# Performance work log

Measured on AMD Instinct MI355X. Metric: run time of the kernel, lower is better.

Reference implementation:

```python
import jax, jax.numpy as jnp
import numpy as np

D_MODEL = 1024
H = 16
D_K = D_MODEL // H


def setup_inputs() -> dict:
    key = jax.random.key(0)
    ks = jax.random.split(key, 12)
    B, S = 2, 2048
    scale = 1.0 / np.sqrt(D_MODEL)
    inp = {
        "q": jax.random.normal(ks[0], (B, S, D_MODEL), jnp.float32),
        "k": jax.random.normal(ks[1], (B, S, D_MODEL), jnp.float32),
        "v": jax.random.normal(ks[2], (B, S, D_MODEL), jnp.float32),
        "mask": jnp.ones((B, 1, S, S), jnp.int32),
        "w_q": jax.random.normal(ks[3], (D_MODEL, D_MODEL), jnp.float32) * scale,
        "b_q": jnp.zeros((D_MODEL,), jnp.float32),
        "w_k": jax.random.normal(ks[4], (D_MODEL, D_MODEL), jnp.float32) * scale,
        "b_k": jnp.zeros((D_MODEL,), jnp.float32),
        "w_v": jax.random.normal(ks[5], (D_MODEL, D_MODEL), jnp.float32) * scale,
        "b_v": jnp.zeros((D_MODEL,), jnp.float32),
        "w_o": jax.random.normal(ks[6], (D_MODEL, D_MODEL), jnp.float32) * scale,
        "b_o": jnp.zeros((D_MODEL,), jnp.float32),
    }
    return inp


def _split_heads(x):
    B, S, _ = x.shape
    return x.reshape(B, S, H, D_K).transpose(0, 2, 1, 3)  # [B,H,S,Dk]


def reference(q, k, v, mask, w_q, b_q, w_k, b_k, w_v, b_v, w_o, b_o):
    # Linear projections (torch Linear: x @ W^T + b)
    query = _split_heads(q @ w_q.T + b_q)
    key = _split_heads(k @ w_k.T + b_k)
    value = _split_heads(v @ w_v.T + b_v)

    # scaled dot-product attention: [B,H,S,S]
    scores = jnp.einsum("bhqd,bhkd->bhqk", query, key) / jnp.sqrt(
        jnp.asarray(D_K, query.dtype)
    )
    scores = jnp.where(mask == 0, jnp.asarray(-1e9, scores.dtype), scores)
    attn = jax.nn.softmax(scores, axis=-1)  # dropout p=0.0 -> identity
    out = jnp.einsum("bhqk,bhkd->bhqd", attn, value)  # [B,H,S,Dk]

    # combine heads -> [B,S,D_MODEL]
    B = out.shape[0]
    out = out.transpose(0, 2, 1, 3).reshape(B, -1, D_MODEL)
    return out @ w_o.T + b_o
```

## Files before the change

### kernel.cpp

```cpp
#include <hip/hip_runtime.h>
#include <hip/hip_bf16.h>

#define S_LEN 2048
#define BATCH 2
#define NH    16
#define DK    64
#define DM    1024

typedef __bf16 bf16x8 __attribute__((ext_vector_type(8)));
typedef float  f32x4  __attribute__((ext_vector_type(4)));
typedef ushort u16x8  __attribute__((ext_vector_type(8)));

__device__ __forceinline__ float bf2f(ushort u) {
    union { unsigned int i; float f; } v; v.i = ((unsigned int)u) << 16; return v.f;
}
__device__ __forceinline__ ushort f2bf(float f) {
    union { float f; unsigned int i; } v; v.f = f;
    unsigned int u = v.i;
    unsigned int r = u + 0x7fff + ((u >> 16) & 1);
    return (ushort)(r >> 16);
}
__device__ __forceinline__ unsigned int packbf(float a, float b) {
    union { float f; unsigned int u; } x, y; x.f = a; y.f = b;
    return (x.u >> 16) | (y.u & 0xFFFF0000u);
}

__device__ __forceinline__ void async_copy16(const ushort* g, ushort* l) {
    __builtin_amdgcn_global_load_lds(
        (__attribute__((address_space(1))) void*)(g),
        (__attribute__((address_space(3))) void*)(l), 16, 0, 0);
}

__global__ void detect(const ushort* __restrict__ q, int* __restrict__ flags) {
    __shared__ int red[256];
    int tid = threadIdx.x;
    int cnt = 0;
    for (int i = tid; i < 2048; i += 256) {
        ushort e = q[2 * i];
        int ex = (e >> 7) & 0xFF;
        if (ex == 0 || (ex >= 107 && ex <= 147)) cnt++;
    }
    red[tid] = cnt;
    __syncthreads();
    for (int s = 128; s > 0; s >>= 1) {
        if (tid < s) red[tid] += red[tid + s];
        __syncthreads();
    }
    if (tid == 0) {
        flags[0] = (red[0] < 1229) ? 1 : 0;
        flags[1] = 0;
    }
}

__global__ void mask_check(const int* __restrict__ mask, int* __restrict__ flags) {
    const int total = BATCH * S_LEN * S_LEN / 4;
    int idx = blockIdx.x * blockDim.x + threadIdx.x;
    int stride = gridDim.x * blockDim.x;
    bool bad = false;
    for (int i = idx; i < total; i += stride) {
        int4 v = ((const int4*)mask)[i];
        if (v.x == 0 || v.y == 0 || v.z == 0 || v.w == 0) bad = true;
    }
    if (__any(bad)) {
        if ((threadIdx.x & 63) == 0) atomicOr(&flags[1], 1);
    }
}

#define NJOBS 11
struct CvtJobs { const void* src[NJOBS]; };

__device__ __constant__ const int g_cum[NJOBS + 1] = {
    0, 4194304, 8388608, 12582912, 13631488, 14680064, 15728640,
    16777216, 16778240, 16779264, 16780288, 16781312
};

__global__ __launch_bounds__(256) void convert_all(CvtJobs J, ushort* __restrict__ conv,
                                                   const int* __restrict__ flags) {
    bool isf32 = flags[0] != 0;
    const int total_chunks = 16781312 / 8;
    int c = blockIdx.x * blockDim.x + threadIdx.x;
    int stride = gridDim.x * blockDim.x;
    for (; c < total_chunks; c += stride) {
        int e = c * 8;
        int j = 0;
        while (j + 1 < NJOBS + 1 && e >= g_cum[j + 1]) j++;
        int local = e - g_cum[j];
        if (isf32) {
            const float* s = (const float*)J.src[j] + local;
            f32x4 a = *(const f32x4*)s;
            f32x4 b = *(const f32x4*)(s + 4);
            ushort o[8] = { f2bf(a[0]), f2bf(a[1]), f2bf(a[2]), f2bf(a[3]),
                            f2bf(b[0]), f2bf(b[1]), f2bf(b[2]), f2bf(b[3]) };
            *(ushort4*)&conv[e]     = *(ushort4*)&o[0];
            *(ushort4*)&conv[e + 4] = *(ushort4*)&o[4];
        } else {
            const ushort* s = (const ushort*)J.src[j] + local;
            bf16x8 v = *(const bf16x8*)s;
            *(bf16x8*)&conv[e] = v;
        }
    }
}

struct GArg { const ushort* x; const ushort* w; const ushort* bias; void* y; int split; float scale; };

__global__ __launch_bounds__(256) void gemm_bt(GArg a0, GArg a1, GArg a2,
                                               const int* __restrict__ flags) {
    GArg A = (blockIdx.z == 0) ? a0 : (blockIdx.z == 1 ? a1 : a2);
    const int K = 1024, N = 1024;
    __shared__ ushort As[2][128 * 32];
    __shared__ ushort Bs[2][128 * 32];

    int tid = threadIdx.x;
    int w = tid >> 6, lane = tid & 63;
    int wm = (w >> 1) * 64, wn = (w & 1) * 64;

    int id = blockIdx.x + 8 * blockIdx.y;
    int m0 = (id & 31) * 128;
    int n0 = (id >> 5) * 128;

    f32x4 acc[4][4] = {};

    int srow0 = w * 16 + (lane >> 2);
    int srow1 = (w + 4) * 16 + (lane >> 2);
    int schunk = ((lane & 3) ^ ((lane >> 3) & 3)) * 8;

    int fr = lane & 15;
    int qd = lane >> 4;
    int fcp = (qd ^ ((fr >> 1) & 3)) * 8;

    const ushort* xr0 = A.x + (size_t)(m0 + srow0) * K + schunk;
    const ushort* xr1 = A.x + (size_t)(m0 + srow1) * K + schunk;
    const ushort* wr0 = A.w + (size_t)(n0 + srow0) * K + schunk;
    const ushort* wr1 = A.w + (size_t)(n0 + srow1) * K + schunk;

    async_copy16(xr0, &As[0][w * 512]);
    async_copy16(xr1, &As[0][(w + 4) * 512]);
    async_copy16(wr0, &Bs[0][w * 512]);
    async_copy16(wr1, &Bs[0][(w + 4) * 512]);

    for (int k = 0; k < 32; k++) {
        __syncthreads();
        int cur = k & 1, nxt = cur ^ 1;

        bf16x8 af[4], bfr[4];
#pragma unroll
        for (int i = 0; i < 4; i++) {
            af[i]  = *(const bf16x8*)&As[cur][(wm + i * 16 + fr) * 32 + fcp];
            bfr[i] = *(const bf16x8*)&Bs[cur][(wn + i * 16 + fr) * 32 + fcp];
        }

        if (k + 1 < 32) {
            int off = (k + 1) * 32;
            async_copy16(xr0 + off, &As[nxt][w * 512]);
            async_copy16(xr1 + off, &As[nxt][(w + 4) * 512]);
            async_copy16(wr0 + off, &Bs[nxt][w * 512]);
            async_copy16(wr1 + off, &Bs[nxt][(w + 4) * 512]);
        }

#pragma unroll
        for (int i = 0; i < 4; i++)
#pragma unroll
            for (int j = 0; j < 4; j++)
                acc[i][j] = __builtin_amdgcn_mfma_f32_16x16x32_bf16(af[i], bfr[j], acc[i][j], 0, 0, 0);
    }

    bool isf32 = flags[0] != 0;
    int crow = qd * 4;
    int ccol = fr;
#pragma unroll
    for (int j = 0; j < 4; j++) {
        int n_g = n0 + wn + j * 16 + ccol;
        float bias = bf2f(A.bias[n_g]);
#pragma unroll
        for (int i = 0; i < 4; i++) {
            if (A.split == 2) {
                ushort4 o;
                o.x = f2bf((acc[i][j][0] + bias) * A.scale);
                o.y = f2bf((acc[i][j][1] + bias) * A.scale);
                o.z = f2bf((acc[i][j][2] + bias) * A.scale);
                o.w = f2bf((acc[i][j][3] + bias) * A.scale);
                int m_g0 = m0 + wm + i * 16 + crow;
                int bb = m_g0 >> 11, s = m_g0 & 2047;
                int h = n_g >> 6, d = n_g & 63;
                *(ushort4*)&((ushort*)A.y)[((size_t)(bb * NH + h) * DK + d) * S_LEN + s] = o;
            } else {
#pragma unroll
                for (int r = 0; r < 4; r++) {
                    int m_g = m0 + wm + i * 16 + crow + r;
                    float val = (acc[i][j][r] + bias) * A.scale;
                    if (A.split) {
                        int bb = m_g >> 11, s = m_g & 2047;
                        int h = n_g >> 6, d = n_g & 63;
                        ((ushort*)A.y)[((size_t)(bb * NH + h) * S_LEN + s) * DK + d] = f2bf(val);
                    } else if (isf32) {
                        ((float*)A.y)[(size_t)m_g * N + n_g] = val;
                    } else {
                        ((ushort*)A.y)[(size_t)m_g * N + n_g] = f2bf(val);
                    }
                }
            }
        }
    }
}

#define PSTR 76

__global__ __launch_bounds__(512, 4) void attn(const ushort* __restrict__ qp,
                                               const ushort* __restrict__ kp,
                                               const ushort* __restrict__ vp,
                                               const int* __restrict__ mask,
                                               const int* __restrict__ flags,
                                               ushort* __restrict__ ctx) {
    __shared__ ushort Ks[2][64 * 64];
    __shared__ ushort Vs[2][64 * 64];
    __shared__ ushort Pb[8][16 * PSTR];

    int tid = threadIdx.x, w = tid >> 6, lane = tid & 63;
    int id = blockIdx.x + 16 * blockIdx.y;
    int bh = id & 31;
    int b = bh >> 4, h = bh & 15;
    int q0 = (id >> 5) * 128;

    const ushort* qb  = qp + (size_t)bh * S_LEN * DK;
    const ushort* kb  = kp + (size_t)bh * S_LEN * DK;
    const ushort* vtb = vp + (size_t)bh * DK * S_LEN;
    const int* mb = mask + (size_t)b * S_LEN * S_LEN;
    bool do_mask = flags[1] != 0;

    int fr = lane & 15;
    int qd = lane >> 4;

    bf16x8 qf[2];
#pragma unroll
    for (int kc = 0; kc < 2; kc++)
        qf[kc] = *(const bf16x8*)&qb[(size_t)(q0 + w * 16 + fr) * DK + kc * 32 + qd * 8];

    bf16x8 ones;
#pragma unroll
    for (int j = 0; j < 8; j++) ones[j] = (__bf16)1.0f;

    f32x4 oacc[4] = {};
    f32x4 lacc = {};

    int srow = w * 8 + (lane >> 3);
    int schunk = ((lane & 7) ^ ((lane >> 3) & 7)) * 8;

    const ushort* kr = kb + (size_t)srow * DK + schunk;
    const ushort* vr = vtb + (size_t)srow * S_LEN + schunk;

    async_copy16(kr, &Ks[0][w * 512]);
    async_copy16(vr, &Vs[0][w * 512]);

    for (int t = 0; t < 32; t++) {
        int k0 = t * 64;
        __syncthreads();
        int cur = t & 1, nxt = cur ^ 1;

        if (t + 1 < 32) {
            int koff = (t + 1) * 64;
            async_copy16(kr + (size_t)koff * DK, &Ks[nxt][w * 512]);
            async_copy16(vr + koff, &Vs[nxt][w * 512]);
        }

        bf16x8 kf[2][4];
#pragma unroll
        for (int kc = 0; kc < 2; kc++)
#pragma unroll
            for (int ct = 0; ct < 4; ct++)
                kf[kc][ct] = *(const bf16x8*)&Ks[cur][(ct * 16 + fr) * 64 + (((kc * 4 + qd) ^ (fr & 7)) * 8)];

        f32x4 sc[4] = {};
        __builtin_amdgcn_s_setprio(1);
#pragma unroll
        for (int kc = 0; kc < 2; kc++)
#pragma unroll
            for (int ct = 0; ct < 4; ct++)
                sc[ct] = __builtin_amdgcn_mfma_f32_16x16x32_bf16(kf[kc][ct], qf[kc], sc[ct], 0, 0, 0);
        __builtin_amdgcn_s_setprio(0);

        if (do_mask) {
            int qr = q0 + w * 16 + fr;
            const int* mrow = &mb[(size_t)qr * S_LEN + k0];
#pragma unroll
            for (int ct = 0; ct < 4; ct++)
#pragma unroll
                for (int r = 0; r < 4; r++)
                    if (mrow[ct * 16 + qd * 4 + r] == 0) sc[ct][r] = -1e9f;
        }

#pragma unroll
        for (int ct = 0; ct < 4; ct++) {
            float p0 = __builtin_amdgcn_exp2f(sc[ct][0]);
            float p1 = __builtin_amdgcn_exp2f(sc[ct][1]);
            float p2 = __builtin_amdgcn_exp2f(sc[ct][2]);
            float p3 = __builtin_amdgcn_exp2f(sc[ct][3]);
            uint2 pk;
            pk.x = packbf(p0, p1);
            pk.y = packbf(p2, p3);
            *(uint2*)&Pb[w][fr * PSTR + ct * 16 + qd * 4] = pk;
        }

        bf16x8 vf[2][4];
#pragma unroll
        for (int kk = 0; kk < 2; kk++)
#pragma unroll
            for (int dt = 0; dt < 4; dt++)
                vf[kk][dt] = *(const bf16x8*)&Vs[cur][(dt * 16 + fr) * 64 + (((kk * 4 + qd) ^ (fr & 7)) * 8)];

        bf16x8 pf[2];
#pragma unroll
        for (int kk = 0; kk < 2; kk++)
            pf[kk] = *(const bf16x8*)&Pb[w][fr * PSTR + kk * 32 + qd * 8];

        __builtin_amdgcn_s_setprio(1);
#pragma unroll
        for (int kk = 0; kk < 2; kk++) {
            lacc = __builtin_amdgcn_mfma_f32_16x16x32_bf16(pf[kk], ones, lacc, 0, 0, 0);
#pragma unroll
            for (int dt = 0; dt < 4; dt++)
                oacc[dt] = __builtin_amdgcn_mfma_f32_16x16x32_bf16(pf[kk], vf[kk][dt], oacc[dt], 0, 0, 0);
        }
        __builtin_amdgcn_s_setprio(0);
    }

#pragma unroll
    for (int r = 0; r < 4; r++) {
        float inv = 1.0f / lacc[r];
        int qr = q0 + w * 16 + qd * 4 + r;
        size_t rowbase = ((size_t)(b * S_LEN + qr) * NH + h) * DK;
#pragma unroll
        for (int dt = 0; dt < 4; dt++)
            ctx[rowbase + dt * 16 + fr] = f2bf(oacc[dt][r] * inv);
    }
}

extern "C" void kernel_launch(void* const* d_in, const int* in_sizes, int n_in,
                              void* d_out, int out_size, void* d_ws, size_t ws_size,
                              hipStream_t stream) {
    const int* mask = (const int*)d_in[3];

    char* ws = (char*)d_ws;
    int*    flags = (int*)ws;
    ushort* conv  = (ushort*)(ws + 4096);
    const size_t conv_bytes = 16781312ull * 2;
    char* p = ws + 4096 + ((conv_bytes + 4095) & ~4095ull);
    size_t sz = (size_t)BATCH * NH * S_LEN * DK * sizeof(ushort);
    ushort* qp  = (ushort*)(p);
    ushort* kp  = (ushort*)(p + sz);
    ushort* vp  = (ushort*)(p + 2 * sz);
    ushort* ctx = (ushort*)(p + 3 * sz);

    ushort* qc  = conv + 0;
    ushort* kc  = conv + 4194304;
    ushort* vc  = conv + 8388608;
    ushort* wqc = conv + 12582912;
    ushort* wkc = conv + 13631488;
    ushort* wvc = conv + 14680064;
    ushort* woc = conv + 15728640;
    ushort* bqc = conv + 16777216;
    ushort* bkc = conv + 16778240;
    ushort* bvc = conv + 16779264;
    ushort* boc = conv + 16780288;

    detect<<<1, 256, 0, stream>>>((const ushort*)d_in[0], flags);
    mask_check<<<1024, 256, 0, stream>>>(mask, flags);

    CvtJobs J;
    J.src[0] = d_in[0];  J.src[1] = d_in[1];  J.src[2] = d_in[2];
    J.src[3] = d_in[4];  J.src[4] = d_in[6];  J.src[5] = d_in[8];
    J.src[6] = d_in[10]; J.src[7] = d_in[5];  J.src[8] = d_in[7];
    J.src[9] = d_in[9];  J.src[10] = d_in[11];
    convert_all<<<2048, 256, 0, stream>>>(J, conv, flags);

    const float cs = 0.125f * 1.44269504f;
    GArg aq{qc, wqc, bqc, qp, 1, cs};
    GArg ak{kc, wkc, bkc, kp, 1, 1.0f};
    GArg av{vc, wvc, bvc, vp, 2, 1.0f};
    gemm_bt<<<dim3(8, 32, 3), 256, 0, stream>>>(aq, ak, av, flags);

    attn<<<dim3(16, 32), 512, 0, stream>>>(qp, kp, vp, mask, flags, ctx);

    GArg ao{ctx, woc, boc, d_out, 0, 1.0f};
    gemm_bt<<<dim3(8, 32, 1), 256, 0, stream>>>(ao, ao, ao, flags);
}
```

Baseline: 256.8 us.

## Split attention over key halves and fuse partial-sum reduction into output GEMM

Attention is split into two key-range halves (flash-decoding style), doubling the grid to 1024 blocks. Each half writes unnormalised fp32 partial outputs and row sums, and the output-projection GEMM now combines and normalises them while staging its A tile. The ones-vector MFMA used for row sums is replaced by a scalar sum of truncated probabilities. The detect and mask_check kernels are folded into convert_all, with a memset of the flags. The cost is extra fp32 partial traffic and synchronous, non-async A loads in the output GEMM.

```diff
diff --git a/kernel.cpp b/kernel.cpp
--- a/kernel.cpp
+++ b/kernel.cpp
@@ -24,6 +24,11 @@
     union { float f; unsigned int u; } x, y; x.f = a; y.f = b;
     return (x.u >> 16) | (y.u & 0xFFFF0000u);
 }
+__device__ __forceinline__ float truncbf(float a) {
+    union { float f; unsigned int u; } x; x.f = a;
+    x.u &= 0xFFFF0000u;
+    return x.f;
+}
 
 __device__ __forceinline__ void async_copy16(const ushort* g, ushort* l) {
     __builtin_amdgcn_global_load_lds(
@@ -31,56 +36,41 @@
         (__attribute__((address_space(3))) void*)(l), 16, 0, 0);
 }
 
-__global__ void detect(const ushort* __restrict__ q, int* __restrict__ flags) {
+#define NJOBS 11
+struct CvtJobs { const void* src[NJOBS]; };
+
+__device__ __constant__ const int g_cum[NJOBS + 1] = {
+    0, 4194304, 8388608, 12582912, 13631488, 14680064, 15728640,
+    16777216, 16778240, 16779264, 16780288, 16781312
+};
+
+__global__ __launch_bounds__(256) void convert_all(CvtJobs J, ushort* __restrict__ conv,
+                                                   const int* __restrict__ mask,
+                                                   int* __restrict__ flags) {
     __shared__ int red[256];
     int tid = threadIdx.x;
-    int cnt = 0;
-    for (int i = tid; i < 2048; i += 256) {
-        ushort e = q[2 * i];
-        int ex = (e >> 7) & 0xFF;
-        if (ex == 0 || (ex >= 107 && ex <= 147)) cnt++;
-    }
-    red[tid] = cnt;
+    {
+        const ushort* q16 = (const ushort*)J.src[0];
+        int cnt = 0;
+        for (int i = tid; i < 2048; i += 256) {
+            ushort e = q16[2 * i];
+            int ex = (e >> 7) & 0xFF;
+            if (ex == 0 || (ex >= 107 && ex <= 147)) cnt++;
+        }
+        red[tid] = cnt;
+    }
     __syncthreads();
     for (int s = 128; s > 0; s >>= 1) {
         if (tid < s) red[tid] += red[tid + s];
         __syncthreads();
     }
-    if (tid == 0) {
-        flags[0] = (red[0] < 1229) ? 1 : 0;
-        flags[1] = 0;
-    }
-}
-
-__global__ void mask_check(const int* __restrict__ mask, int* __restrict__ flags) {
-    const int total = BATCH * S_LEN * S_LEN / 4;
-    int idx = blockIdx.x * blockDim.x + threadIdx.x;
+    bool isf32 = red[0] < 1229;
+    if (blockIdx.x == 0 && tid == 0) flags[0] = isf32 ? 1 : 0;
+
+    const int total_chunks = 16781312 / 8;
+    int idx = blockIdx.x * blockDim.x + tid;
     int stride = gridDim.x * blockDim.x;
-    bool bad = false;
-    for (int i = idx; i < total; i += stride) {
-        int4 v = ((const int4*)mask)[i];
-        if (v.x == 0 || v.y == 0 || v.z == 0 || v.w == 0) bad = true;
-    }
-    if (__any(bad)) {
-        if ((threadIdx.x & 63) == 0) atomicOr(&flags[1], 1);
-    }
-}
-
-#define NJOBS 11
-struct CvtJobs { const void* src[NJOBS]; };
-
-__device__ __constant__ const int g_cum[NJOBS + 1] = {
-    0, 4194304, 8388608, 12582912, 13631488, 14680064, 15728640,
-    16777216, 16778240, 16779264, 16780288, 16781312
-};
-
-__global__ __launch_bounds__(256) void convert_all(CvtJobs J, ushort* __restrict__ conv,
-                                                   const int* __restrict__ flags) {
-    bool isf32 = flags[0] != 0;
-    const int total_chunks = 16781312 / 8;
-    int c = blockIdx.x * blockDim.x + threadIdx.x;
-    int stride = gridDim.x * blockDim.x;
-    for (; c < total_chunks; c += stride) {
+    for (int c = idx; c < total_chunks; c += stride) {
         int e = c * 8;
         int j = 0;
         while (j + 1 < NJOBS + 1 && e >= g_cum[j + 1]) j++;
@@ -99,9 +89,47 @@
             *(bf16x8*)&conv[e] = v;
         }
     }
+    const int4* m4 = (const int4*)mask;
+    bool bad = false;
+    for (int c = idx; c < 2097152; c += stride) {
+        int4 v = m4[c];
+        if (v.x == 0 || v.y == 0 || v.z == 0 || v.w == 0) bad = true;
+    }
+    if (__any(bad)) {
+        if ((tid & 63) == 0) atomicOr(&flags[1], 1);
+    }
 }
 
 struct GArg { const ushort* x; const ushort* w; const ushort* bias; void* y; int split; float scale; };
+
+__device__ __forceinline__ void stage_fused(ushort* dstA, const float* op, const float* lp,
+                                            int m0, int w, int lane, int kk) {
+    int schunk = ((lane & 3) ^ ((lane >> 3) & 3)) * 8;
+    int kcol = kk * 32 + schunk;
+    int h = kcol >> 6, dcol = kcol & 63;
+#pragma unroll
+    for (int half = 0; half < 2; half++) {
+        int srow = (half ? (w + 4) : w) * 16 + (lane >> 2);
+        int m_g = m0 + srow;
+        int bb = m_g >> 11, s = m_g & 2047;
+        size_t prow = (size_t)(bb * 16 + h) * 2048 + s;
+        const float* p0 = op + prow * 64 + dcol;
+        const float* p1 = p0 + 4194304;
+        f32x4 a0 = *(const f32x4*)p0;
+        f32x4 a1 = *(const f32x4*)(p0 + 4);
+        f32x4 c0 = *(const f32x4*)p1;
+        f32x4 c1 = *(const f32x4*)(p1 + 4);
+        float inv = 1.0f / (lp[prow] + lp[prow + 65536]);
+        ushort o[8];
+#pragma unroll
+        for (int j = 0; j < 4; j++) o[j]     = f2bf((a0[j] + c0[j]) * inv);
+#pragma unroll
+        for (int j = 0; j < 4; j++) o[4 + j] = f2bf((a1[j] + c1[j]) * inv);
+        ushort* dst = dstA + (half ? (w + 4) : w) * 512 + lane * 8;
+        *(ushort4*)dst       = *(ushort4*)&o[0];
+        *(ushort4*)(dst + 4) = *(ushort4*)&o[4];
+    }
+}
 
 __global__ __launch_bounds__(256) void gemm_bt(GArg a0, GArg a1, GArg a2,
                                                const int* __restrict__ flags) {
@@ -118,6 +146,10 @@
     int m0 = (id & 31) * 128;
     int n0 = (id >> 5) * 128;
 
+    bool fuseA = (A.split == 3);
+    const float* opf = (const float*)A.x;
+    const float* lpf = opf + 8388608;
+
     f32x4 acc[4][4] = {};
 
     int srow0 = w * 16 + (lane >> 2);
@@ -133,8 +165,12 @@
     const ushort* wr0 = A.w + (size_t)(n0 + srow0) * K + schunk;
     const ushort* wr1 = A.w + (size_t)(n0 + srow1) * K + schunk;
 
-    async_copy16(xr0, &As[0][w * 512]);
-    async_copy16(xr1, &As[0][(w + 4) * 512]);
+    if (fuseA) {
+        stage_fused(&As[0][0], opf, lpf, m0, w, lane, 0);
+    } else {
+        async_copy16(xr0, &As[0][w * 512]);
+        async_copy16(xr1, &As[0][(w + 4) * 512]);
+    }
     async_copy16(wr0, &Bs[0][w * 512]);
     async_copy16(wr1, &Bs[0][(w + 4) * 512]);
 
@@ -151,8 +187,12 @@
 
         if (k + 1 < 32) {
             int off = (k + 1) * 32;
-            async_copy16(xr0 + off, &As[nxt][w * 512]);
-            async_copy16(xr1 + off, &As[nxt][(w + 4) * 512]);
+            if (fuseA) {
+                stage_fused(&As[nxt][0], opf, lpf, m0, w, lane, k + 1);
+            } else {
+                async_copy16(xr0 + off, &As[nxt][w * 512]);
+                async_copy16(xr1 + off, &As[nxt][(w + 4) * 512]);
+            }
             async_copy16(wr0 + off, &Bs[nxt][w * 512]);
             async_copy16(wr1 + off, &Bs[nxt][(w + 4) * 512]);
         }
@@ -183,16 +223,21 @@
                 int bb = m_g0 >> 11, s = m_g0 & 2047;
                 int h = n_g >> 6, d = n_g & 63;
                 *(ushort4*)&((ushort*)A.y)[((size_t)(bb * NH + h) * DK + d) * S_LEN + s] = o;
-            } else {
+            } else if (A.split == 1) {
 #pragma unroll
                 for (int r = 0; r < 4; r++) {
                     int m_g = m0 + wm + i * 16 + crow + r;
                     float val = (acc[i][j][r] + bias) * A.scale;
-                    if (A.split) {
-                        int bb = m_g >> 11, s = m_g & 2047;
-                        int h = n_g >> 6, d = n_g & 63;
-                        ((ushort*)A.y)[((size_t)(bb * NH + h) * S_LEN + s) * DK + d] = f2bf(val);
-                    } else if (isf32) {
+                    int bb = m_g >> 11, s = m_g & 2047;
+                    int h = n_g >> 6, d = n_g & 63;
+                    ((ushort*)A.y)[((size_t)(bb * NH + h) * S_LEN + s) * DK + d] = f2bf(val);
+                }
+            } else {
+#pragma unroll
+                for (int r = 0; r < 4; r++) {
+                    int m_g = m0 + wm + i * 16 + crow + r;
+                    float val = (acc[i][j][r] + bias) * A.scale;
+                    if (isf32) {
                         ((float*)A.y)[(size_t)m_g * N + n_g] = val;
                     } else {
                         ((ushort*)A.y)[(size_t)m_g * N + n_g] = f2bf(val);
@@ -205,21 +250,25 @@
 
 #define PSTR 76
 
-__global__ __launch_bounds__(512, 4) void attn(const ushort* __restrict__ qp,
+__global__ __launch_bounds__(512, 6) void attn(const ushort* __restrict__ qp,
                                                const ushort* __restrict__ kp,
                                                const ushort* __restrict__ vp,
                                                const int* __restrict__ mask,
                                                const int* __restrict__ flags,
-                                               ushort* __restrict__ ctx) {
+                                               float* __restrict__ opart,
+                                               float* __restrict__ lpart) {
     __shared__ ushort Ks[2][64 * 64];
     __shared__ ushort Vs[2][64 * 64];
     __shared__ ushort Pb[8][16 * PSTR];
 
     int tid = threadIdx.x, w = tid >> 6, lane = tid & 63;
-    int id = blockIdx.x + 16 * blockIdx.y;
+    int id = blockIdx.x + 32 * blockIdx.y;
     int bh = id & 31;
-    int b = bh >> 4, h = bh & 15;
-    int q0 = (id >> 5) * 128;
+    int b = bh >> 4;
+    int rest = id >> 5;
+    int q0 = (rest & 15) * 128;
+    int ks = rest >> 4;
+    int kbase = ks * 1024;
 
     const ushort* qb  = qp + (size_t)bh * S_LEN * DK;
     const ushort* kb  = kp + (size_t)bh * S_LEN * DK;
@@ -235,28 +284,23 @@
     for (int kc = 0; kc < 2; kc++)
         qf[kc] = *(const bf16x8*)&qb[(size_t)(q0 + w * 16 + fr) * DK + kc * 32 + qd * 8];
 
-    bf16x8 ones;
-#pragma unroll
-    for (int j = 0; j < 8; j++) ones[j] = (__bf16)1.0f;
-
     f32x4 oacc[4] = {};
-    f32x4 lacc = {};
+    float llocal = 0.0f;
 
     int srow = w * 8 + (lane >> 3);
     int schunk = ((lane & 7) ^ ((lane >> 3) & 7)) * 8;
 
-    const ushort* kr = kb + (size_t)srow * DK + schunk;
-    const ushort* vr = vtb + (size_t)srow * S_LEN + schunk;
+    const ushort* kr = kb + (size_t)(kbase + srow) * DK + schunk;
+    const ushort* vr = vtb + (size_t)srow * S_LEN + kbase + schunk;
 
     async_copy16(kr, &Ks[0][w * 512]);
     async_copy16(vr, &Vs[0][w * 512]);
 
-    for (int t = 0; t < 32; t++) {
-        int k0 = t * 64;
+    for (int t = 0; t < 16; t++) {
         __syncthreads();
         int cur = t & 1, nxt = cur ^ 1;
 
-        if (t + 1 < 32) {
+        if (t + 1 < 16) {
             int koff = (t + 1) * 64;
             async_copy16(kr + (size_t)koff * DK, &Ks[nxt][w * 512]);
             async_copy16(vr + koff, &Vs[nxt][w * 512]);
@@ -280,7 +324,7 @@
 
         if (do_mask) {
             int qr = q0 + w * 16 + fr;
-            const int* mrow = &mb[(size_t)qr * S_LEN + k0];
+            const int* mrow = &mb[(size_t)qr * S_LEN + kbase + t * 64];
 #pragma unroll
             for (int ct = 0; ct < 4; ct++)
 #pragma unroll
@@ -298,6 +342,7 @@
             pk.x = packbf(p0, p1);
             pk.y = packbf(p2, p3);
             *(uint2*)&Pb[w][fr * PSTR + ct * 16 + qd * 4] = pk;
+            llocal += (truncbf(p0) + truncbf(p1)) + (truncbf(p2) + truncbf(p3));
         }
 
         bf16x8 vf[2][4];
@@ -314,24 +359,24 @@
 
         __builtin_amdgcn_s_setprio(1);
 #pragma unroll
-        for (int kk = 0; kk < 2; kk++) {
-            lacc = __builtin_amdgcn_mfma_f32_16x16x32_bf16(pf[kk], ones, lacc, 0, 0, 0);
+        for (int kk = 0; kk < 2; kk++)
 #pragma unroll
             for (int dt = 0; dt < 4; dt++)
                 oacc[dt] = __builtin_amdgcn_mfma_f32_16x16x32_bf16(pf[kk], vf[kk][dt], oacc[dt], 0, 0, 0);
-        }
         __builtin_amdgcn_s_setprio(0);
     }
 
-#pragma unroll
-    for (int r = 0; r < 4; r++) {
-        float inv = 1.0f / lacc[r];
-        int qr = q0 + w * 16 + qd * 4 + r;
-        size_t rowbase = ((size_t)(b * S_LEN + qr) * NH + h) * DK;
-#pragma unroll
-        for (int dt = 0; dt < 4; dt++)
-            ctx[rowbase + dt * 16 + fr] = f2bf(oacc[dt][r] * inv);
-    }
+    llocal += __shfl_xor(llocal, 16);
+    llocal += __shfl_xor(llocal, 32);
+    if (qd == 0)
+        lpart[(size_t)ks * 65536 + (size_t)bh * S_LEN + (q0 + w * 16 + fr)] = llocal;
+
+    size_t obase = ((size_t)(ks * 32 + bh) * S_LEN + (q0 + w * 16)) * DK;
+#pragma unroll
+    for (int dt = 0; dt < 4; dt++)
+#pragma unroll
+        for (int r = 0; r < 4; r++)
+            opart[obase + (size_t)(qd * 4 + r) * DK + dt * 16 + fr] = oacc[dt][r];
 }
 
 extern "C" void kernel_launch(void* const* d_in, const int* in_sizes, int n_in,
@@ -348,7 +393,8 @@
     ushort* qp  = (ushort*)(p);
     ushort* kp  = (ushort*)(p + sz);
     ushort* vp  = (ushort*)(p + 2 * sz);
-    ushort* ctx = (ushort*)(p + 3 * sz);
+    float*  opart = (float*)(p + 4 * sz);
+    float*  lpart = (float*)(p + 4 * sz + 2 * (size_t)BATCH * NH * S_LEN * DK * sizeof(float));
 
     ushort* qc  = conv + 0;
     ushort* kc  = conv + 4194304;
@@ -362,15 +408,14 @@
     ushort* bvc = conv + 16779264;
     ushort* boc = conv + 16780288;
 
-    detect<<<1, 256, 0, stream>>>((const ushort*)d_in[0], flags);
-    mask_check<<<1024, 256, 0, stream>>>(mask, flags);
+    hipMemsetAsync(flags, 0, 2 * sizeof(int), stream);
 
     CvtJobs J;
     J.src[0] = d_in[0];  J.src[1] = d_in[1];  J.src[2] = d_in[2];
     J.src[3] = d_in[4];  J.src[4] = d_in[6];  J.src[5] = d_in[8];
     J.src[6] = d_in[10]; J.src[7] = d_in[5];  J.src[8] = d_in[7];
     J.src[9] = d_in[9];  J.src[10] = d_in[11];
-    convert_all<<<2048, 256, 0, stream>>>(J, conv, flags);
+    convert_all<<<2048, 256, 0, stream>>>(J, conv, mask, flags);
 
     const float cs = 0.125f * 1.44269504f;
     GArg aq{qc, wqc, bqc, qp, 1, cs};
@@ -378,8 +423,8 @@
     GArg av{vc, wvc, bvc, vp, 2, 1.0f};
     gemm_bt<<<dim3(8, 32, 3), 256, 0, stream>>>(aq, ak, av, flags);
 
-    attn<<<dim3(16, 32), 512, 0, stream>>>(qp, kp, vp, mask, flags, ctx);
-
-    GArg ao{ctx, woc, boc, d_out, 0, 1.0f};
+    attn<<<dim3(32, 32), 512, 0, stream>>>(qp, kp, vp, mask, flags, opart, lpart);
+
+    GArg ao{(const ushort*)opart, woc, boc, d_out, 3, 1.0f};
     gemm_bt<<<dim3(8, 32, 1), 256, 0, stream>>>(ao, ao, ao, flags);
 }
```

New measurement: 304.6 us. +18.6%, slower.
